# Kernel optimization log

Hardware: AMD Instinct MI355X
Metric: run time of the kernel (lower is better)

## Reference

```python
import jax, jax.numpy as jnp
import numpy as np

PI = 3.141592653589
RMAX = 6.0
RMIN = 0.5
NBASIS = 25
B, NATOM, MNBR = 8, 256, 100


def setup_inputs() -> dict:
    key = jax.random.key(0)
    ks = jax.random.split(key, 10)
    Imagetype = jax.random.randint(ks[0], (B, NATOM), 1, 5)
    neighbor_list = jax.random.randint(ks[1], (B, NATOM, MNBR), 0, NATOM + 1)
    # rij in (0.2, 7.0): some neighbors fall outside the 6.0 cutoff
    r = jax.random.uniform(ks[2], (B, NATOM, MNBR), minval=0.2, maxval=7.0)
    xyz = jax.random.normal(ks[3], (B, NATOM, MNBR, 3))
    xyz = xyz / (jnp.linalg.norm(xyz, axis=-1, keepdims=True) + 1e-6) * r[..., None]
    ImagedR = jnp.concatenate([r[..., None], xyz], axis=-1)  # [B,N,M,4]
    n_embed = 0.1 + 0.2 * jax.random.normal(ks[4], (40, 5))
    W1 = 0.04 * jax.random.normal(ks[5], (100, 625)); b1 = jnp.zeros((100,))
    W2 = 0.10 * jax.random.normal(ks[6], (100, 100)); b2 = jnp.zeros((100,))
    W3 = 0.10 * jax.random.normal(ks[7], (100, 100)); b3 = jnp.zeros((100,))
    W4 = 0.10 * jax.random.normal(ks[8], (1, 100)); b4 = 3.3 + jax.random.normal(ks[9], (1,))
    return dict(Imagetype=Imagetype, neighbor_list=neighbor_list, ImagedR=ImagedR,
                n_embed=n_embed, W1=W1, b1=b1, W2=W2, b2=b2, W3=W3, b3=b3, W4=W4, b4=b4)


def _moment(ImagedR):
    # radial basis fc and its analytic d(fc)/dr projected onto x,y,z directions
    rij = ImagedR[..., 0]            # [B,N,M]
    xyz = ImagedR[..., 1:4]          # [B,N,M,3]
    rs = jnp.linspace(RMIN, RMAX, NBASIS)
    r = rij[..., None]               # [B,N,M,1] broadcast vs rs -> [B,N,M,25]
    cond = (r < RMAX) & (r > 0)
    gauss = jnp.exp(-(r - rs) ** 2)
    cut = 0.5 * jnp.cos(PI * r) + 0.5
    fc = jnp.where(cond, gauss * cut, 0.0)
    dfc = jnp.where(cond, gauss * (-2.0 * (r - rs)) * cut - gauss * 0.5 * PI * jnp.sin(PI * r), 0.0)
    unit = jnp.where(rij[..., None] != 0, xyz / rij[..., None], 0.0)   # [B,N,M,3]
    dfeat = unit[:, :, :, None, :] * dfc[..., None]                    # [B,N,M,25,3]
    return fc, dfeat


def _energy(feat, Imagetype, neighbor_list, n_embed, W1, b1, W2, b2, W3, b3, W4, b4):
    b, n, m, k = feat.shape
    # type of each neighbor; index 0 (no neighbor) -> type 0
    padded = jnp.concatenate([jnp.zeros((b, 1), Imagetype.dtype), Imagetype], axis=1)  # [B,N+1]
    nbr_type = padded[jnp.arange(b)[:, None, None], neighbor_list]                     # [B,N,M]
    iit = n_embed[Imagetype]        # [B,N,5]
    jjt = n_embed[nbr_type]         # [B,N,M,5]
    emb = (iit[:, :, None, :, None] * jjt[:, :, :, None, :]).reshape(b, n, m, 25)
    # outer(feat_k, emb_e) summed over neighbors -> [B,N,25,25]
    G = jnp.einsum('bnmk,bnme->bnke', feat, emb).reshape(b, n, 625)
    x1 = G @ W1.T + b1
    x3 = jnp.tanh(x1) @ W2.T + b2 + x1
    x5 = jnp.tanh(x3) @ W3.T + b3 + x3
    Ei = jnp.tanh(x5) @ W4.T + b4   # [B,N,1]
    Etot = Ei.sum(axis=1)           # [B,1]
    return Etot, Ei


def reference(Imagetype, neighbor_list, ImagedR, n_embed, W1, b1, W2, b2, W3, b3, W4, b4):
    b, n, m = neighbor_list.shape
    feat, dfeat = _moment(ImagedR)
    Etot, Ei = _energy(feat, Imagetype, neighbor_list, n_embed, W1, b1, W2, b2, W3, b3, W4, b4)
    # dE/dfeat with ones cotangent on Etot (== grad of sum)
    dE = jax.grad(lambda f: _energy(f, Imagetype, neighbor_list, n_embed,
                                    W1, b1, W2, b2, W3, b3, W4, b4)[0].sum())(feat)  # [B,N,M,25]
    dE_Rid = jnp.einsum('bnmk,bnmkd->bnmd', dE, dfeat)  # [B,N,M,3]
    Force = -dE_Rid.sum(axis=2)                         # [B,N,3]
    # scatter-add reaction forces onto neighbor atoms (1-based ids, 0 = padding)
    buf = jnp.zeros((b, n + 1, 3), dE_Rid.dtype).at[
        jnp.arange(b)[:, None, None], neighbor_list].add(dE_Rid)
    Force = Force + buf[:, 1:]
    return Etot, Ei, Force
```

## Files before the change

### kernel.cpp

```cpp
#include <hip/hip_runtime.h>
#include <math.h>

#define PI_F 3.14159274f
#define STEP (5.5f/24.0f)

constexpr int BATCH = 8;
constexpr int NATOM = 256;
constexpr int MNBR  = 100;
constexpr int NB    = 25;
constexpr int NATOT = BATCH * NATOM;
constexpr int ABLK  = 4;
constexpr int NMBLK = NATOT / ABLK;
constexpr int PPB   = NMBLK / BATCH;

constexpr int OFF_W1T  = 0;
constexpr int OFF_W1TT = 62500;
constexpr int OFF_W2T  = 125000;
constexpr int OFF_W3T  = 135000;
constexpr int OFF_PART = 145000;
constexpr size_t WS_NEED = (size_t)(OFF_PART + NMBLK * 768) * 4;

__global__ __launch_bounds__(128)
void k_prep(const float* __restrict__ nemb, const float* __restrict__ W1,
            const float* __restrict__ W2, const float* __restrict__ W3,
            float* __restrict__ ws)
{
    int bid = blockIdx.x, tid = threadIdx.x;
    if (bid < 500) {
        int t = bid / 100, jo = bid - (bid / 100) * 100;
        if (tid < 125) {
            int k = tid / 5, j = tid - (tid / 5) * 5;
            float s = 0.f;
            #pragma unroll
            for (int i = 0; i < 5; i++)
                s = fmaf(W1[jo * 625 + k * 25 + i * 5 + j], nemb[t * 5 + i], s);
            ws[OFF_W1T  + (t * 100 + jo) * 125 + tid] = s;
            ws[OFF_W1TT + t * 12500 + tid * 100 + jo] = s;
        }
    } else {
        int jo = bid - 500;
        if (tid < 100) {
            ws[OFF_W2T + tid * 100 + jo] = W2[jo * 100 + tid];
            ws[OFF_W3T + tid * 100 + jo] = W3[jo * 100 + tid];
        }
    }
}

template<bool USE_PART>
__global__ __launch_bounds__(512)
void k_main(const int* __restrict__ itype, const int* __restrict__ nbr,
            const float* __restrict__ imdR, const float* __restrict__ nemb,
            const float* __restrict__ b1, const float* __restrict__ b2,
            const float* __restrict__ b3, const float* __restrict__ W4,
            const float* __restrict__ b4,
            float* __restrict__ ws, float* __restrict__ out)
{
    int base = blockIdx.x * ABLK;
    int b    = base >> 8;
    int tid  = threadIdx.x;

    __shared__ float r_s[400], cut_s[400], sin_s[400];
    __shared__ float x_s[400], y_s[400], z_s[400];
    __shared__ int   nb_s[400];
    __shared__ float jjt_s[2000];
    __shared__ float H_s[500];
    __shared__ float x1_s[400], t1_s[400], x3_s[400], t3_s[400], t5_s[400];
    __shared__ float g5_s[400], g3_s[400], g1_s[400];
    __shared__ float fbuf[NATOM * 3];
    __shared__ int   t_s[4];

    if (tid < 4) t_s[tid] = itype[base + tid];
    for (int q = tid; q < NATOM * 3; q += 512) fbuf[q] = 0.f;
    if (tid < 400) {
        int a = tid / 100, m = tid - (tid / 100) * 100;
        int atom = base + a;
        float4 v = *reinterpret_cast<const float4*>(imdR + ((size_t)atom * MNBR + m) * 4);
        float r = v.x;
        r_s[tid] = r;
        float sc, cc; sincosf(PI_F * r, &sc, &cc);
        bool cond = (r < 6.0f && r > 0.0f);
        cut_s[tid] = cond ? (0.5f * cc + 0.5f) : 0.f;
        sin_s[tid] = cond ? sc : 0.f;
        x_s[tid] = v.y; y_s[tid] = v.z; z_s[tid] = v.w;
        int j = nbr[atom * MNBR + m];
        nb_s[tid] = j;
        int tj = (j > 0) ? itype[b * NATOM + (j - 1)] : 0;
        #pragma unroll
        for (int q = 0; q < 5; q++) jjt_s[tid * 5 + q] = nemb[tj * 5 + q];
    }
    __syncthreads();

    if (tid < 500) {
        int a = tid / 125, q = tid - (tid / 125) * 125;
        int k = q / 5, j = q - (q / 5) * 5;
        float rs = 0.5f + k * STEP;
        int am0 = a * 100;
        float acc = 0.f;
        for (int m = 0; m < MNBR; m++) {
            float r = r_s[am0 + m];
            float d = r - rs;
            float g = expf(-d * d);
            acc = fmaf(g * cut_s[am0 + m], jjt_s[(am0 + m) * 5 + j], acc);
        }
        H_s[tid] = acc;
    }
    __syncthreads();

    if (tid < 400) {
        int a = tid / 100, jo = tid - (tid / 100) * 100;
        const float* wt = ws + OFF_W1TT + t_s[a] * 12500;
        const float* hh = H_s + a * 125;
        float acc = 0.f;
        for (int q = 0; q < 125; q++) acc = fmaf(wt[q * 100 + jo], hh[q], acc);
        float v = acc + b1[jo];
        x1_s[tid] = v; t1_s[tid] = tanhf(v);
    }
    __syncthreads();

    if (tid < 400) {
        int a = tid / 100, jo = tid - (tid / 100) * 100;
        const float* wt = ws + OFF_W2T;
        const float* tt = t1_s + a * 100;
        float acc = 0.f;
        for (int k = 0; k < 100; k++) acc = fmaf(wt[k * 100 + jo], tt[k], acc);
        float v = acc + b2[jo] + x1_s[tid];
        x3_s[tid] = v; t3_s[tid] = tanhf(v);
    }
    __syncthreads();

    if (tid < 400) {
        int a = tid / 100, jo = tid - (tid / 100) * 100;
        const float* wt = ws + OFF_W3T;
        const float* tt = t3_s + a * 100;
        float acc = 0.f;
        for (int k = 0; k < 100; k++) acc = fmaf(wt[k * 100 + jo], tt[k], acc);
        float v = acc + b3[jo] + x3_s[tid];
        t5_s[tid] = tanhf(v);
    }
    __syncthreads();

    if (tid < 256) {
        int a = tid >> 6, lane = tid & 63;
        float acc = 0.f;
        for (int j = lane; j < 100; j += 64) acc += t5_s[a * 100 + j] * W4[j];
        #pragma unroll
        for (int mm = 32; mm > 0; mm >>= 1) acc += __shfl_xor(acc, mm, 64);
        if (lane == 0) out[8 + base + a] = acc + b4[0];
    }
    if (tid < 400) {
        int jo = tid - (tid / 100) * 100;
        float t = t5_s[tid];
        g5_s[tid] = W4[jo] * (1.f - t * t);
    }
    __syncthreads();

    if (tid < 400) {
        int a = tid / 100, k = tid - (tid / 100) * 100;
        const float* gg = g5_s + a * 100;
        const float* wt = ws + OFF_W3T + k * 100;
        float acc = 0.f;
        for (int j = 0; j < 100; j++) acc = fmaf(wt[j], gg[j], acc);
        float t = t3_s[tid];
        g3_s[tid] = g5_s[tid] + (1.f - t * t) * acc;
    }
    __syncthreads();

    if (tid < 400) {
        int a = tid / 100, k = tid - (tid / 100) * 100;
        const float* gg = g3_s + a * 100;
        const float* wt = ws + OFF_W2T + k * 100;
        float acc = 0.f;
        for (int j = 0; j < 100; j++) acc = fmaf(wt[j], gg[j], acc);
        float t = t1_s[tid];
        g1_s[tid] = g3_s[tid] + (1.f - t * t) * acc;
    }
    __syncthreads();

    if (tid < 500) {
        int a = tid / 125, q = tid - (tid / 125) * 125;
        const float* wt = ws + OFF_W1T + t_s[a] * 12500;
        const float* gg = g1_s + a * 100;
        float acc = 0.f;
        for (int jo = 0; jo < 100; jo++) acc = fmaf(wt[jo * 125 + q], gg[jo], acc);
        H_s[tid] = acc;
    }
    __syncthreads();

    {
        int w = tid >> 6, lane = tid & 63;
        int a = w >> 1, h = w & 1;
        float d0 = 0.f, d1 = 0.f, d2 = 0.f;
        if (lane < 50) {
            int am = a * 100 + h * 50 + lane;
            float r = r_s[am], cut = cut_s[am];
            float sterm = 0.5f * PI_F * sin_s[am];
            float j0 = jjt_s[am*5+0], j1v = jjt_s[am*5+1], j2 = jjt_s[am*5+2],
                  j3 = jjt_s[am*5+3], j4 = jjt_s[am*5+4];
            const float* dh0 = H_s + a * 125;
            float s = 0.f;
            for (int k = 0; k < NB; k++) {
                const float* dh = dh0 + k * 5;
                float dE = j0*dh[0] + j1v*dh[1] + j2*dh[2] + j3*dh[3] + j4*dh[4];
                float d  = r - (0.5f + k * STEP);
                float g  = expf(-d * d);
                float dfc = g * (-2.f * d) * cut - g * sterm;
                s = fmaf(dE, dfc, s);
            }
            float inv = (r != 0.f) ? 1.f / r : 0.f;
            d0 = s * x_s[am] * inv; d1 = s * y_s[am] * inv; d2 = s * z_s[am] * inv;
            int j = nb_s[am];
            if (j > 0) {
                atomicAdd(&fbuf[(j - 1) * 3 + 0], d0);
                atomicAdd(&fbuf[(j - 1) * 3 + 1], d1);
                atomicAdd(&fbuf[(j - 1) * 3 + 2], d2);
            }
        }
        #pragma unroll
        for (int mm = 32; mm > 0; mm >>= 1) {
            d0 += __shfl_xor(d0, mm, 64);
            d1 += __shfl_xor(d1, mm, 64);
            d2 += __shfl_xor(d2, mm, 64);
        }
        if (lane == 0) {
            int tl = (base + a) & 255;
            atomicAdd(&fbuf[tl * 3 + 0], -d0);
            atomicAdd(&fbuf[tl * 3 + 1], -d1);
            atomicAdd(&fbuf[tl * 3 + 2], -d2);
        }
    }
    __syncthreads();

    if (USE_PART) {
        for (int q = tid; q < NATOM * 3; q += 512)
            ws[OFF_PART + (size_t)blockIdx.x * 768 + q] = fbuf[q];
    } else {
        for (int q = tid; q < NATOM * 3; q += 512) {
            float vq = fbuf[q];
            if (vq != 0.f) atomicAdd(&out[8 + NATOT + (b << 8) * 3 + q], vq);
        }
    }
}

__global__ __launch_bounds__(256)
void k_red(const float* __restrict__ ws, float* __restrict__ out, int nfblk)
{
    int bid = blockIdx.x, tid = threadIdx.x;
    if (bid < nfblk) {
        int idx = bid * 256 + tid;
        int b = idx / 768, q = idx - b * 768;
        float s = 0.f;
        #pragma unroll 8
        for (int p = 0; p < PPB; p++)
            s += ws[OFF_PART + (size_t)(b * PPB + p) * 768 + q];
        out[8 + NATOT + idx] = s;
    } else {
        int e = bid - nfblk;
        float v = out[8 + e * 256 + tid];
        #pragma unroll
        for (int mm = 32; mm > 0; mm >>= 1) v += __shfl_xor(v, mm, 64);
        __shared__ float wsum[4];
        if ((tid & 63) == 0) wsum[tid >> 6] = v;
        __syncthreads();
        if (tid == 0) out[e] = wsum[0] + wsum[1] + wsum[2] + wsum[3];
    }
}

extern "C" void kernel_launch(void* const* d_in, const int* in_sizes, int n_in,
                              void* d_out, int out_size, void* d_ws, size_t ws_size,
                              hipStream_t stream)
{
    (void)in_sizes; (void)n_in;

    const int*   itype = (const int*)  d_in[0];
    const int*   nbr   = (const int*)  d_in[1];
    const float* imdR  = (const float*)d_in[2];
    const float* nemb  = (const float*)d_in[3];
    const float* W1    = (const float*)d_in[4];
    const float* b1    = (const float*)d_in[5];
    const float* W2    = (const float*)d_in[6];
    const float* b2    = (const float*)d_in[7];
    const float* W3    = (const float*)d_in[8];
    const float* b3    = (const float*)d_in[9];
    const float* W4    = (const float*)d_in[10];
    const float* b4    = (const float*)d_in[11];

    float* out = (float*)d_out;
    float* ws  = (float*)d_ws;

    bool use_part = ws_size >= WS_NEED;
    if (!use_part)
        hipMemsetAsync((char*)d_out + (size_t)(8 + NATOT) * 4, 0,
                       (size_t)NATOT * 3 * 4, stream);

    hipLaunchKernelGGL(k_prep, dim3(600), dim3(128), 0, stream,
                       nemb, W1, W2, W3, ws);
    if (use_part) {
        hipLaunchKernelGGL((k_main<true>), dim3(NMBLK), dim3(512), 0, stream,
                           itype, nbr, imdR, nemb, b1, b2, b3, W4, b4, ws, out);
        hipLaunchKernelGGL(k_red, dim3(32), dim3(256), 0, stream, ws, out, 24);
    } else {
        hipLaunchKernelGGL((k_main<false>), dim3(NMBLK), dim3(512), 0, stream,
                           itype, nbr, imdR, nemb, b1, b2, b3, W4, b4, ws, out);
        hipLaunchKernelGGL(k_red, dim3(8), dim3(256), 0, stream, ws, out, 0);
    }
}
```

Measured before the change: 136.5 us.

## Split feature accumulation across neighbor chunks and use multiple accumulators in matvecs

The H computation now runs one thread per (chunk, atom, basis) over 25 neighbors, with five embedding accumulators per thread. The gaussian is computed once per neighbor instead of once per embedding column, and partials are reduced through a shared scratch buffer that also replaces the gradient arrays. All dense matvec loops use several independent accumulators to break the FMA dependency chains, and expf is replaced with the faster, less accurate __expf. This adds one extra sync and reduction stage and slightly changes floating-point summation order.

```diff
diff --git a/kernel.cpp b/kernel.cpp
--- a/kernel.cpp
+++ b/kernel.cpp
@@ -65,9 +65,13 @@
     __shared__ float jjt_s[2000];
     __shared__ float H_s[500];
     __shared__ float x1_s[400], t1_s[400], x3_s[400], t3_s[400], t5_s[400];
-    __shared__ float g5_s[400], g3_s[400], g1_s[400];
+    __shared__ float scratch[2000];
     __shared__ float fbuf[NATOM * 3];
     __shared__ int   t_s[4];
+
+    float* g5_s = scratch;
+    float* g3_s = scratch + 500;
+    float* g1_s = scratch + 1000;
 
     if (tid < 4) t_s[tid] = itype[base + tid];
     for (int q = tid; q < NATOM * 3; q += 512) fbuf[q] = 0.f;
@@ -90,51 +94,78 @@
     }
     __syncthreads();
 
-    if (tid < 500) {
-        int a = tid / 125, q = tid - (tid / 125) * 125;
-        int k = q / 5, j = q - (q / 5) * 5;
+    if (tid < 400) {
+        int c = tid / 100, rem = tid - (tid / 100) * 100;
+        int a = rem / 25, k = rem - (rem / 25) * 25;
         float rs = 0.5f + k * STEP;
-        int am0 = a * 100;
-        float acc = 0.f;
-        for (int m = 0; m < MNBR; m++) {
-            float r = r_s[am0 + m];
-            float d = r - rs;
-            float g = expf(-d * d);
-            acc = fmaf(g * cut_s[am0 + m], jjt_s[(am0 + m) * 5 + j], acc);
-        }
-        H_s[tid] = acc;
-    }
+        int am0 = a * 100 + c * 25;
+        float ac0 = 0.f, ac1 = 0.f, ac2 = 0.f, ac3 = 0.f, ac4 = 0.f;
+        for (int m = 0; m < 25; m++) {
+            int am = am0 + m;
+            float d = r_s[am] - rs;
+            float g = __expf(-d * d) * cut_s[am];
+            const float* jj = jjt_s + am * 5;
+            ac0 = fmaf(g, jj[0], ac0);
+            ac1 = fmaf(g, jj[1], ac1);
+            ac2 = fmaf(g, jj[2], ac2);
+            ac3 = fmaf(g, jj[3], ac3);
+            ac4 = fmaf(g, jj[4], ac4);
+        }
+        float* pp = scratch + tid * 5;
+        pp[0] = ac0; pp[1] = ac1; pp[2] = ac2; pp[3] = ac3; pp[4] = ac4;
+    }
+    __syncthreads();
+
+    if (tid < 500)
+        H_s[tid] = (scratch[tid] + scratch[500 + tid])
+                 + (scratch[1000 + tid] + scratch[1500 + tid]);
     __syncthreads();
 
     if (tid < 400) {
         int a = tid / 100, jo = tid - (tid / 100) * 100;
-        const float* wt = ws + OFF_W1TT + t_s[a] * 12500;
+        const float* wt = ws + OFF_W1TT + t_s[a] * 12500 + jo;
         const float* hh = H_s + a * 125;
-        float acc = 0.f;
-        for (int q = 0; q < 125; q++) acc = fmaf(wt[q * 100 + jo], hh[q], acc);
-        float v = acc + b1[jo];
+        float a0 = 0.f, a1 = 0.f, a2 = 0.f, a3 = 0.f, a4 = 0.f;
+        for (int q = 0; q < 125; q += 5) {
+            a0 = fmaf(wt[(q + 0) * 100], hh[q + 0], a0);
+            a1 = fmaf(wt[(q + 1) * 100], hh[q + 1], a1);
+            a2 = fmaf(wt[(q + 2) * 100], hh[q + 2], a2);
+            a3 = fmaf(wt[(q + 3) * 100], hh[q + 3], a3);
+            a4 = fmaf(wt[(q + 4) * 100], hh[q + 4], a4);
+        }
+        float v = ((a0 + a1) + (a2 + a3)) + a4 + b1[jo];
         x1_s[tid] = v; t1_s[tid] = tanhf(v);
     }
     __syncthreads();
 
     if (tid < 400) {
         int a = tid / 100, jo = tid - (tid / 100) * 100;
-        const float* wt = ws + OFF_W2T;
+        const float* wt = ws + OFF_W2T + jo;
         const float* tt = t1_s + a * 100;
-        float acc = 0.f;
-        for (int k = 0; k < 100; k++) acc = fmaf(wt[k * 100 + jo], tt[k], acc);
-        float v = acc + b2[jo] + x1_s[tid];
+        float a0 = 0.f, a1 = 0.f, a2 = 0.f, a3 = 0.f;
+        for (int k = 0; k < 100; k += 4) {
+            a0 = fmaf(wt[(k + 0) * 100], tt[k + 0], a0);
+            a1 = fmaf(wt[(k + 1) * 100], tt[k + 1], a1);
+            a2 = fmaf(wt[(k + 2) * 100], tt[k + 2], a2);
+            a3 = fmaf(wt[(k + 3) * 100], tt[k + 3], a3);
+        }
+        float v = (a0 + a1) + (a2 + a3) + b2[jo] + x1_s[tid];
         x3_s[tid] = v; t3_s[tid] = tanhf(v);
     }
     __syncthreads();
 
     if (tid < 400) {
         int a = tid / 100, jo = tid - (tid / 100) * 100;
-        const float* wt = ws + OFF_W3T;
+        const float* wt = ws + OFF_W3T + jo;
         const float* tt = t3_s + a * 100;
-        float acc = 0.f;
-        for (int k = 0; k < 100; k++) acc = fmaf(wt[k * 100 + jo], tt[k], acc);
-        float v = acc + b3[jo] + x3_s[tid];
+        float a0 = 0.f, a1 = 0.f, a2 = 0.f, a3 = 0.f;
+        for (int k = 0; k < 100; k += 4) {
+            a0 = fmaf(wt[(k + 0) * 100], tt[k + 0], a0);
+            a1 = fmaf(wt[(k + 1) * 100], tt[k + 1], a1);
+            a2 = fmaf(wt[(k + 2) * 100], tt[k + 2], a2);
+            a3 = fmaf(wt[(k + 3) * 100], tt[k + 3], a3);
+        }
+        float v = (a0 + a1) + (a2 + a3) + b3[jo] + x3_s[tid];
         t5_s[tid] = tanhf(v);
     }
     __syncthreads();
@@ -158,10 +189,15 @@
         int a = tid / 100, k = tid - (tid / 100) * 100;
         const float* gg = g5_s + a * 100;
         const float* wt = ws + OFF_W3T + k * 100;
-        float acc = 0.f;
-        for (int j = 0; j < 100; j++) acc = fmaf(wt[j], gg[j], acc);
+        float a0 = 0.f, a1 = 0.f, a2 = 0.f, a3 = 0.f;
+        for (int j = 0; j < 100; j += 4) {
+            a0 = fmaf(wt[j + 0], gg[j + 0], a0);
+            a1 = fmaf(wt[j + 1], gg[j + 1], a1);
+            a2 = fmaf(wt[j + 2], gg[j + 2], a2);
+            a3 = fmaf(wt[j + 3], gg[j + 3], a3);
+        }
         float t = t3_s[tid];
-        g3_s[tid] = g5_s[tid] + (1.f - t * t) * acc;
+        g3_s[tid] = g5_s[tid] + (1.f - t * t) * ((a0 + a1) + (a2 + a3));
     }
     __syncthreads();
 
@@ -169,20 +205,30 @@
         int a = tid / 100, k = tid - (tid / 100) * 100;
         const float* gg = g3_s + a * 100;
         const float* wt = ws + OFF_W2T + k * 100;
-        float acc = 0.f;
-        for (int j = 0; j < 100; j++) acc = fmaf(wt[j], gg[j], acc);
+        float a0 = 0.f, a1 = 0.f, a2 = 0.f, a3 = 0.f;
+        for (int j = 0; j < 100; j += 4) {
+            a0 = fmaf(wt[j + 0], gg[j + 0], a0);
+            a1 = fmaf(wt[j + 1], gg[j + 1], a1);
+            a2 = fmaf(wt[j + 2], gg[j + 2], a2);
+            a3 = fmaf(wt[j + 3], gg[j + 3], a3);
+        }
         float t = t1_s[tid];
-        g1_s[tid] = g3_s[tid] + (1.f - t * t) * acc;
+        g1_s[tid] = g3_s[tid] + (1.f - t * t) * ((a0 + a1) + (a2 + a3));
     }
     __syncthreads();
 
     if (tid < 500) {
         int a = tid / 125, q = tid - (tid / 125) * 125;
-        const float* wt = ws + OFF_W1T + t_s[a] * 12500;
+        const float* wt = ws + OFF_W1T + t_s[a] * 12500 + q;
         const float* gg = g1_s + a * 100;
-        float acc = 0.f;
-        for (int jo = 0; jo < 100; jo++) acc = fmaf(wt[jo * 125 + q], gg[jo], acc);
-        H_s[tid] = acc;
+        float a0 = 0.f, a1 = 0.f, a2 = 0.f, a3 = 0.f;
+        for (int jo = 0; jo < 100; jo += 4) {
+            a0 = fmaf(wt[(jo + 0) * 125], gg[jo + 0], a0);
+            a1 = fmaf(wt[(jo + 1) * 125], gg[jo + 1], a1);
+            a2 = fmaf(wt[(jo + 2) * 125], gg[jo + 2], a2);
+            a3 = fmaf(wt[(jo + 3) * 125], gg[jo + 3], a3);
+        }
+        H_s[tid] = (a0 + a1) + (a2 + a3);
     }
     __syncthreads();
 
@@ -202,7 +248,7 @@
                 const float* dh = dh0 + k * 5;
                 float dE = j0*dh[0] + j1v*dh[1] + j2*dh[2] + j3*dh[3] + j4*dh[4];
                 float d  = r - (0.5f + k * STEP);
-                float g  = expf(-d * d);
+                float g  = __expf(-d * d);
                 float dfc = g * (-2.f * d) * cut - g * sterm;
                 s = fmaf(dE, dfc, s);
             }
```

Measured after the change: 122.5 us. 10.3% less time.
